# Optimization experiments

Measured on AMD Instinct MI355X. Metric: run time of the kernel, lower is better.

Reference implementation:

```python
import jax, jax.numpy as jnp
import numpy as np

B, LQ, LK = 8, 512, 512
DQ = DK = DV = 512
H = 128


def setup_inputs() -> dict:
    key = jax.random.key(0)
    kq, kk, kv, k1, k2, k3 = jax.random.split(key, 6)
    query = jax.random.normal(kq, (B, LQ, DQ), dtype=jnp.float32)
    key_t = jax.random.normal(kk, (B, LK, DK), dtype=jnp.float32)
    value = jax.random.normal(kv, (B, LK, DV), dtype=jnp.float32)
    # Linear weights stored torch-style as (out_features, in_features)
    w1 = jax.random.normal(k1, (H, DQ), dtype=jnp.float32) / np.sqrt(DQ)
    w2 = jax.random.normal(k2, (H, DK), dtype=jnp.float32) / np.sqrt(DK)
    v = jax.random.normal(k3, (1, H), dtype=jnp.float32) / np.sqrt(H)
    return {"query": query, "key": key_t, "value": value, "w1": w1, "w2": w2, "v": v}


def reference(query, key, value, w1, w2, v):
    # Linear projections first (mathematically identical to projecting the
    # broadcast tensors, since Linear is linear): (B,Lq,H), (B,Lk,H)
    q_proj = jnp.einsum("bqd,hd->bqh", query, w1)
    k_proj = jnp.einsum("bkd,hd->bkh", key, w2)
    # Broadcast add -> tanh -> project to scalar: (B,Lq,Lk,H) intermediate
    feat = jnp.tanh(q_proj[:, :, None, :] + k_proj[:, None, :, :])
    score = jnp.einsum("bqkh,h->bqk", feat, v[0])
    attention_weights = jax.nn.softmax(score, axis=-1)
    context_vector = jnp.einsum("bqk,bkv->bqv", attention_weights, value)
    return (attention_weights, context_vector)
```

## Files before the change

### kernel.cpp

```cpp
#include <hip/hip_runtime.h>

#define TWO_LOG2E 2.8853900817779268f

__device__ __forceinline__ float frcp(float x) {
#if __has_builtin(__builtin_amdgcn_rcpf)
  return __builtin_amdgcn_rcpf(x);
#else
  return 1.0f / x;
#endif
}
__device__ __forceinline__ float fexp2(float x) {
#if __has_builtin(__builtin_amdgcn_exp2f)
  return __builtin_amdgcn_exp2f(x);
#else
  return exp2f(x);
#endif
}
__device__ __forceinline__ unsigned short f2bf(float f) {
  unsigned int u = __float_as_uint(f);
  u += 0x7fffu + ((u >> 16) & 1u);
  return (unsigned short)(u >> 16);
}
__device__ __forceinline__ unsigned int pack2bf(float lo, float hi) {
  return (unsigned int)f2bf(lo) | ((unsigned int)f2bf(hi) << 16);
}

using short8 = __attribute__((ext_vector_type(8))) short;
using f32x4v = __attribute__((ext_vector_type(4))) float;
using f32x8s = __attribute__((ext_vector_type(8))) float;
using f32x2 = __attribute__((ext_vector_type(2))) float;

__device__ __forceinline__ f32x2 pkfma(f32x2 a, f32x2 b, f32x2 c) {
  return __builtin_elementwise_fma(a, b, c);
}
__device__ __forceinline__ f32x2 splat2(float x) {
  f32x2 r;
  r.x = x;
  r.y = x;
  return r;
}
__device__ __forceinline__ f32x2 unpack_bf2(unsigned u) {
  f32x2 r;
  r.x = __uint_as_float(u << 16);
  r.y = __uint_as_float(u & 0xffff0000u);
  return r;
}
__device__ __forceinline__ void cell4k(float a0, float a1, float a2, float a3,
                                       f32x2 b0, f32x2 b1, f32x2 b2, f32x2 b3,
                                       float v0, float v1, float v2, float v3,
                                       f32x2& s) {
  const f32x2 one = {1.f, 1.f};
  f32x2 x0 = pkfma(splat2(a0), b0, one);
  f32x2 x1 = pkfma(splat2(a1), b1, one);
  f32x2 x2 = pkfma(splat2(a2), b2, one);
  f32x2 x3 = pkfma(splat2(a3), b3, one);
  f32x2 p01 = x0 * x1, p23 = x2 * x3;
  f32x2 n01 = pkfma(splat2(v0), x1, splat2(v1) * x0);
  f32x2 n23 = pkfma(splat2(v2), x3, splat2(v3) * x2);
  f32x2 num = pkfma(n01, p23, n23 * p01);
  f32x2 den = p01 * p23;
  f32x2 r;
  r.x = frcp(den.x);
  r.y = frcp(den.y);
  s = pkfma(num, r, s);
}

__global__ __launch_bounds__(256) void k_pre(
    const float* __restrict__ query, const float* __restrict__ key,
    const float* __restrict__ w1, const float* __restrict__ w2,
    const float* __restrict__ value,
    float* __restrict__ Aout, unsigned short* __restrict__ BoutT,
    unsigned short* __restrict__ valT) {
  __shared__ __align__(16) char Abuf[16 * 128];
  __shared__ __align__(16) char Bbuf[128 * 128];
  __shared__ unsigned short ts[64][66];

  const int t = threadIdx.x;

  if (blockIdx.y == 0) {
    const int px = blockIdx.x;
    const bool isB = px >= 256;
    const float* in = isB ? key : query;
    const float* wm = isB ? w2 : w1;
    const int m0g = (px & 255) * 16;
    const int w = t >> 6, l = t & 63;

    f32x4v acc[2];
    acc[0] = 0;
    acc[1] = 0;

    float4 aS;
    float4 wS[4][2];

#define P_LOAD(k0_)                                                        \
  {                                                                        \
    aS = *(const float4*)&in[(m0g + (t >> 4)) * 512 + (k0_) + (t & 15) * 4]; \
    _Pragma("unroll") for (int i = 0; i < 4; ++i) {                        \
      int tt = t + i * 256;                                                \
      int row = tt >> 3, g = tt & 7;                                       \
      const float* src = &wm[row * 512 + (k0_) + g * 8];                   \
      wS[i][0] = *(const float4*)src;                                      \
      wS[i][1] = *(const float4*)(src + 4);                                \
    }                                                                      \
  }
#define P_WRITE()                                                          \
  {                                                                        \
    int arow = t >> 4, q4 = t & 15;                                        \
    *(uint2*)(Abuf + arow * 128 + (((q4 >> 1) ^ (arow & 7)) << 4) +        \
              ((q4 & 1) << 3)) =                                           \
        make_uint2(pack2bf(aS.x, aS.y), pack2bf(aS.z, aS.w));              \
    _Pragma("unroll") for (int i = 0; i < 4; ++i) {                        \
      int tt = t + i * 256;                                                \
      int row = tt >> 3, g = tt & 7;                                       \
      uint4 p = make_uint4(                                                \
          pack2bf(wS[i][0].x, wS[i][0].y), pack2bf(wS[i][0].z, wS[i][0].w),\
          pack2bf(wS[i][1].x, wS[i][1].y), pack2bf(wS[i][1].z, wS[i][1].w));\
      *(uint4*)(Bbuf + row * 128 + ((g ^ (row & 7)) << 4)) = p;            \
    }                                                                      \
  }

    P_LOAD(0);
#pragma unroll
    for (int ks8 = 0; ks8 < 8; ++ks8) {
      if (ks8) __syncthreads();
      P_WRITE();
      if (ks8 < 7) P_LOAD(ks8 * 64 + 64);
      __syncthreads();
#pragma unroll
      for (int ks = 0; ks < 2; ++ks) {
        const int gb = ks * 4 + (l >> 4);
        const int ra = l & 15;
        short8 af = *(const short8*)(Abuf + ra * 128 + ((gb ^ (ra & 7)) << 4));
#pragma unroll
        for (int ni = 0; ni < 2; ++ni) {
          const int rb = w * 32 + ni * 16 + (l & 15);
          short8 bf_ = *(const short8*)(Bbuf + rb * 128 + ((gb ^ (rb & 7)) << 4));
          if (isB)
            acc[ni] = __builtin_amdgcn_mfma_f32_16x16x32_bf16(bf_, af, acc[ni], 0, 0, 0);
          else
            acc[ni] = __builtin_amdgcn_mfma_f32_16x16x32_bf16(af, bf_, acc[ni], 0, 0, 0);
        }
      }
    }
#undef P_LOAD
#undef P_WRITE
    if (!isB) {
#pragma unroll
      for (int ni = 0; ni < 2; ++ni) {
        int col = w * 32 + ni * 16 + (l & 15);
#pragma unroll
        for (int j = 0; j < 4; ++j) {
          int row = m0g + (l >> 4) * 4 + j;
          Aout[row * 128 + col] = fexp2(acc[ni][j] * TWO_LOG2E);
        }
      }
    } else {
      int m = m0g + (l & 15);
#pragma unroll
      for (int ni = 0; ni < 2; ++ni)
#pragma unroll
        for (int j = 0; j < 4; ++j) {
          int h = w * 32 + ni * 16 + (l >> 4) * 4 + j;
          BoutT[h * 4096 + m] = f2bf(fexp2(acc[ni][j] * TWO_LOG2E));
        }
    }
  } else {
    const int x = blockIdx.x;
    const int b = x >> 6, k0 = ((x >> 3) & 7) * 64, n0 = (x & 7) * 64;
    {
      int kr = t >> 4, n4 = (t & 15) * 4;
#pragma unroll
      for (int i = 0; i < 4; ++i) {
        float4 f =
            *(const float4*)&value[((b * 512) + k0 + kr + 16 * i) * 512 + n0 + n4];
        *(ushort4*)&ts[kr + 16 * i][n4] =
            make_ushort4(f2bf(f.x), f2bf(f.y), f2bf(f.z), f2bf(f.w));
      }
    }
    __syncthreads();
    {
      int nw = t >> 4, k4 = (t & 15) * 4;
#pragma unroll
      for (int i = 0; i < 4; ++i) {
        int n = nw + 16 * i;
        ushort4 o = make_ushort4(ts[k4 + 0][n], ts[k4 + 1][n], ts[k4 + 2][n],
                                 ts[k4 + 3][n]);
        *(ushort4*)&valT[((b * 512) + n0 + n) * 512 + k0 + k4] = o;
      }
    }
  }
}

__global__ __launch_bounds__(256, 4) void k_score_softmax(
    const float* __restrict__ Aexp, const unsigned short* __restrict__ BexpT,
    const float* __restrict__ vw, float* __restrict__ attn) {
  __shared__ float red[4][4];

  const int tid = threadIdx.x;
  const int b = blockIdx.y;
  const int qbase = blockIdx.x * 4;
  const int wav = tid >> 6;
  const int lane = tid & 63;

  const unsigned* const bbase32 = (const unsigned*)(BexpT + b * 512);
  const int kidx = wav * 64 + lane;

  const float* const pa0 =
      Aexp + __builtin_amdgcn_readfirstlane((b * 512 + qbase) * 128);
  const float* const pa1 = pa0 + 128;
  const float* const pa2 = pa0 + 256;
  const float* const pa3 = pa0 + 384;
  const float* const pv = vw;

  f32x2 acc0 = {0.f, 0.f}, acc1 = {0.f, 0.f};
  f32x2 acc2 = {0.f, 0.f}, acc3 = {0.f, 0.f};

#pragma unroll
  for (int ch = 0; ch < 16; ++ch) {
    f32x8s sa0, sa1, sa2, sa3, sv;
    unsigned soff = (unsigned)(ch * 32);
    asm volatile(
        "s_load_dwordx8 %0, %5, %10\n\t"
        "s_load_dwordx8 %1, %6, %10\n\t"
        "s_load_dwordx8 %2, %7, %10\n\t"
        "s_load_dwordx8 %3, %8, %10\n\t"
        "s_load_dwordx8 %4, %9, %10"
        : "=&s"(sa0), "=&s"(sa1), "=&s"(sa2), "=&s"(sa3), "=&s"(sv)
        : "s"(pa0), "s"(pa1), "s"(pa2), "s"(pa3), "s"(pv), "s"(soff));

    unsigned u[8];
#pragma unroll
    for (int j = 0; j < 8; ++j)
      u[j] = bbase32[ch * 16384 + j * 2048 + kidx];

    asm volatile("s_waitcnt lgkmcnt(0)"
                 : "+s"(sa0), "+s"(sa1), "+s"(sa2), "+s"(sa3), "+s"(sv));

#pragma unroll
    for (int g = 0; g < 2; ++g) {
      f32x2 b0 = unpack_bf2(u[g * 4 + 0]);
      f32x2 b1 = unpack_bf2(u[g * 4 + 1]);
      f32x2 b2 = unpack_bf2(u[g * 4 + 2]);
      f32x2 b3 = unpack_bf2(u[g * 4 + 3]);
      const int h = g * 4;
      cell4k(sa0[h], sa0[h + 1], sa0[h + 2], sa0[h + 3], b0, b1, b2, b3,
             sv[h], sv[h + 1], sv[h + 2], sv[h + 3], acc0);
      cell4k(sa1[h], sa1[h + 1], sa1[h + 2], sa1[h + 3], b0, b1, b2, b3,
             sv[h], sv[h + 1], sv[h + 2], sv[h + 3], acc1);
      cell4k(sa2[h], sa2[h + 1], sa2[h + 2], sa2[h + 3], b0, b1, b2, b3,
             sv[h], sv[h + 1], sv[h + 2], sv[h + 3], acc2);
      cell4k(sa3[h], sa3[h + 1], sa3[h + 2], sa3[h + 3], b0, b1, b2, b3,
             sv[h], sv[h + 1], sv[h + 2], sv[h + 3], acc3);
    }
  }

  float P0e = fexp2(acc0.x * -TWO_LOG2E);
  float P0o = fexp2(acc0.y * -TWO_LOG2E);
  float P1e = fexp2(acc1.x * -TWO_LOG2E);
  float P1o = fexp2(acc1.y * -TWO_LOG2E);
  float P2e = fexp2(acc2.x * -TWO_LOG2E);
  float P2o = fexp2(acc2.y * -TWO_LOG2E);
  float P3e = fexp2(acc3.x * -TWO_LOG2E);
  float P3o = fexp2(acc3.y * -TWO_LOG2E);
  float s0 = P0e + P0o, s1 = P1e + P1o, s2 = P2e + P2o, s3 = P3e + P3o;
#pragma unroll
  for (int off = 32; off > 0; off >>= 1) {
    s0 += __shfl_xor(s0, off);
    s1 += __shfl_xor(s1, off);
    s2 += __shfl_xor(s2, off);
    s3 += __shfl_xor(s3, off);
  }
  if (lane == 0) {
    red[wav][0] = s0; red[wav][1] = s1; red[wav][2] = s2; red[wav][3] = s3;
  }
  __syncthreads();
  float r0 = frcp(red[0][0] + red[1][0] + red[2][0] + red[3][0]);
  float r1 = frcp(red[0][1] + red[1][1] + red[2][1] + red[3][1]);
  float r2 = frcp(red[0][2] + red[1][2] + red[2][2] + red[3][2]);
  float r3 = frcp(red[0][3] + red[1][3] + red[2][3] + red[3][3]);

  const int row0 = (b * 512 + qbase) * 512;
  const int k0 = kidx * 2;
  *(float2*)&attn[row0 + k0] = make_float2(P0e * r0, P0o * r0);
  *(float2*)&attn[row0 + 512 + k0] = make_float2(P1e * r1, P1o * r1);
  *(float2*)&attn[row0 + 1024 + k0] = make_float2(P2e * r2, P2o * r2);
  *(float2*)&attn[row0 + 1536 + k0] = make_float2(P3e * r3, P3o * r3);
}

__global__ __launch_bounds__(256) void k_context_mfma(
    const float* __restrict__ attn, const unsigned short* __restrict__ valT,
    float* __restrict__ ctx) {
  __shared__ __align__(16) char At[64 * 128];
  __shared__ __align__(16) char Bt[64 * 128];

  const int t = threadIdx.x;
  const int b = blockIdx.z;
  const int m0 = blockIdx.y * 64, n0 = blockIdx.x * 64;
  const int w = t >> 6, l = t & 63;
  const int wr = w >> 1, wc = w & 1;

  f32x4v acc[2][2];
  acc[0][0] = 0; acc[0][1] = 0; acc[1][0] = 0; acc[1][1] = 0;

  const int sr = t >> 2;
  const int sg = (t & 3);
  const int sswz = sr & 7;

  for (int k0 = 0; k0 < 512; k0 += 64) {
    if (k0) __syncthreads();
    {
      const float* src = &attn[(b * 512 + m0 + sr) * 512 + k0 + sg * 16];
      char* dst = At + sr * 128;
#pragma unroll
      for (int h = 0; h < 2; ++h) {
        float4 f0 = *(const float4*)(src + h * 8);
        float4 f1 = *(const float4*)(src + h * 8 + 4);
        uint4 p = make_uint4(pack2bf(f0.x, f0.y), pack2bf(f0.z, f0.w),
                             pack2bf(f1.x, f1.y), pack2bf(f1.z, f1.w));
        int g = sg * 2 + h;
        *(uint4*)(dst + ((g ^ sswz) << 4)) = p;
      }
      const unsigned short* srcb = &valT[(b * 512 + n0 + sr) * 512 + k0];
      char* dstb = Bt + sr * 128;
#pragma unroll
      for (int h = 0; h < 2; ++h) {
        int g = sg + h * 4;
        uint4 vb = *(const uint4*)(srcb + g * 8);
        *(uint4*)(dstb + ((g ^ sswz) << 4)) = vb;
      }
    }
    __syncthreads();
#pragma unroll
    for (int ks = 0; ks < 2; ++ks) {
      const int gb = ks * 4 + (l >> 4);
      short8 af[2], bf_[2];
#pragma unroll
      for (int mi = 0; mi < 2; ++mi) {
        int ra = wr * 32 + mi * 16 + (l & 15);
        af[mi] = *(const short8*)(At + ra * 128 + ((gb ^ (ra & 7)) << 4));
      }
#pragma unroll
      for (int ni = 0; ni < 2; ++ni) {
        int rb = wc * 32 + ni * 16 + (l & 15);
        bf_[ni] = *(const short8*)(Bt + rb * 128 + ((gb ^ (rb & 7)) << 4));
      }
#pragma unroll
      for (int mi = 0; mi < 2; ++mi)
#pragma unroll
        for (int ni = 0; ni < 2; ++ni)
          acc[mi][ni] = __builtin_amdgcn_mfma_f32_16x16x32_bf16(
              af[mi], bf_[ni], acc[mi][ni], 0, 0, 0);
    }
  }
  __syncthreads();
#pragma unroll
  for (int mi = 0; mi < 2; ++mi)
#pragma unroll
    for (int ni = 0; ni < 2; ++ni) {
      int col = n0 + wc * 32 + ni * 16 + (l & 15);
#pragma unroll
      for (int j = 0; j < 4; ++j) {
        int row = m0 + wr * 32 + mi * 16 + (l >> 4) * 4 + j;
        ctx[(b * 512 + row) * 512 + col] = acc[mi][ni][j];
      }
    }
}

extern "C" void kernel_launch(void* const* d_in, const int* in_sizes, int n_in,
                              void* d_out, int out_size, void* d_ws, size_t ws_size,
                              hipStream_t stream) {
  const float* query = (const float*)d_in[0];
  const float* key   = (const float*)d_in[1];
  const float* value = (const float*)d_in[2];
  const float* w1    = (const float*)d_in[3];
  const float* w2    = (const float*)d_in[4];
  const float* v     = (const float*)d_in[5];

  float* attn = (float*)d_out;
  float* ctx  = attn + 8 * 512 * 512;

  float* Aexp = (float*)d_ws;
  unsigned short* BexpT = (unsigned short*)(Aexp + 4096 * 128);
  unsigned short* valT = BexpT + 128 * 4096;

  k_pre<<<dim3(512, 2), 256, 0, stream>>>(query, key, w1, w2, value,
                                          Aexp, BexpT, valT);
  k_score_softmax<<<dim3(128, 8), 256, 0, stream>>>(Aexp, BexpT, v, attn);
  k_context_mfma<<<dim3(8, 8, 8), 256, 0, stream>>>(attn, valT, ctx);
}
```

Baseline: 60.35 us.

## Split score kernel's hidden-dim reduction across two wave groups per block

The score/softmax kernel now launches 512 threads per block. Two groups of four waves each reduce half of the 128 hidden dimensions, then the partial sums are combined through shared memory. Each group writes two of the four query rows. This halves the serial per-thread accumulation chain and doubles resident waves to hide memory latency. The cost is an extra LDS exchange, a barrier, redundant exp work, and tighter register limits under the new launch bounds.

```diff
diff --git a/kernel.cpp b/kernel.cpp
--- a/kernel.cpp
+++ b/kernel.cpp
@@ -191,19 +191,22 @@
   }
 }
 
-__global__ __launch_bounds__(256, 4) void k_score_softmax(
+__global__ __launch_bounds__(512, 8) void k_score_softmax(
     const float* __restrict__ Aexp, const unsigned short* __restrict__ BexpT,
     const float* __restrict__ vw, float* __restrict__ attn) {
-  __shared__ float red[4][4];
+  __shared__ __align__(16) f32x2 part[512][4];
+  __shared__ float red[8][4];
 
   const int tid = threadIdx.x;
   const int b = blockIdx.y;
   const int qbase = blockIdx.x * 4;
   const int wav = tid >> 6;
+  const int hgrp = wav >> 2;
+  const int kq = wav & 3;
   const int lane = tid & 63;
 
   const unsigned* const bbase32 = (const unsigned*)(BexpT + b * 512);
-  const int kidx = wav * 64 + lane;
+  const int kidx = kq * 64 + lane;
 
   const float* const pa0 =
       Aexp + __builtin_amdgcn_readfirstlane((b * 512 + qbase) * 128);
@@ -211,14 +214,15 @@
   const float* const pa2 = pa0 + 256;
   const float* const pa3 = pa0 + 384;
   const float* const pv = vw;
+  const unsigned hoff = (unsigned)__builtin_amdgcn_readfirstlane(hgrp * 256);
 
   f32x2 acc0 = {0.f, 0.f}, acc1 = {0.f, 0.f};
   f32x2 acc2 = {0.f, 0.f}, acc3 = {0.f, 0.f};
 
 #pragma unroll
-  for (int ch = 0; ch < 16; ++ch) {
+  for (int ch = 0; ch < 8; ++ch) {
     f32x8s sa0, sa1, sa2, sa3, sv;
-    unsigned soff = (unsigned)(ch * 32);
+    unsigned soff = hoff + (unsigned)(ch * 32);
     asm volatile(
         "s_load_dwordx8 %0, %5, %10\n\t"
         "s_load_dwordx8 %1, %6, %10\n\t"
@@ -231,7 +235,7 @@
     unsigned u[8];
 #pragma unroll
     for (int j = 0; j < 8; ++j)
-      u[j] = bbase32[ch * 16384 + j * 2048 + kidx];
+      u[j] = bbase32[hgrp * 131072 + ch * 16384 + j * 2048 + kidx];
 
     asm volatile("s_waitcnt lgkmcnt(0)"
                  : "+s"(sa0), "+s"(sa1), "+s"(sa2), "+s"(sa3), "+s"(sv));
@@ -254,6 +258,19 @@
     }
   }
 
+  part[tid][0] = acc0;
+  part[tid][1] = acc1;
+  part[tid][2] = acc2;
+  part[tid][3] = acc3;
+  __syncthreads();
+  {
+    const f32x2* pp = part[tid ^ 256];
+    acc0 += pp[0];
+    acc1 += pp[1];
+    acc2 += pp[2];
+    acc3 += pp[3];
+  }
+
   float P0e = fexp2(acc0.x * -TWO_LOG2E);
   float P0o = fexp2(acc0.y * -TWO_LOG2E);
   float P1e = fexp2(acc1.x * -TWO_LOG2E);
@@ -274,17 +291,21 @@
     red[wav][0] = s0; red[wav][1] = s1; red[wav][2] = s2; red[wav][3] = s3;
   }
   __syncthreads();
-  float r0 = frcp(red[0][0] + red[1][0] + red[2][0] + red[3][0]);
-  float r1 = frcp(red[0][1] + red[1][1] + red[2][1] + red[3][1]);
-  float r2 = frcp(red[0][2] + red[1][2] + red[2][2] + red[3][2]);
-  float r3 = frcp(red[0][3] + red[1][3] + red[2][3] + red[3][3]);
+  const int rb = hgrp * 4;
+  float r0 = frcp(red[rb][0] + red[rb + 1][0] + red[rb + 2][0] + red[rb + 3][0]);
+  float r1 = frcp(red[rb][1] + red[rb + 1][1] + red[rb + 2][1] + red[rb + 3][1]);
+  float r2 = frcp(red[rb][2] + red[rb + 1][2] + red[rb + 2][2] + red[rb + 3][2]);
+  float r3 = frcp(red[rb][3] + red[rb + 1][3] + red[rb + 2][3] + red[rb + 3][3]);
 
   const int row0 = (b * 512 + qbase) * 512;
   const int k0 = kidx * 2;
-  *(float2*)&attn[row0 + k0] = make_float2(P0e * r0, P0o * r0);
-  *(float2*)&attn[row0 + 512 + k0] = make_float2(P1e * r1, P1o * r1);
-  *(float2*)&attn[row0 + 1024 + k0] = make_float2(P2e * r2, P2o * r2);
-  *(float2*)&attn[row0 + 1536 + k0] = make_float2(P3e * r3, P3o * r3);
+  if (hgrp == 0) {
+    *(float2*)&attn[row0 + k0] = make_float2(P0e * r0, P0o * r0);
+    *(float2*)&attn[row0 + 512 + k0] = make_float2(P1e * r1, P1o * r1);
+  } else {
+    *(float2*)&attn[row0 + 1024 + k0] = make_float2(P2e * r2, P2o * r2);
+    *(float2*)&attn[row0 + 1536 + k0] = make_float2(P3e * r3, P3o * r3);
+  }
 }
 
 __global__ __launch_bounds__(256) void k_context_mfma(
@@ -385,6 +406,6 @@
 
   k_pre<<<dim3(512, 2), 256, 0, stream>>>(query, key, w1, w2, value,
                                           Aexp, BexpT, valT);
-  k_score_softmax<<<dim3(128, 8), 256, 0, stream>>>(Aexp, BexpT, v, attn);
+  k_score_softmax<<<dim3(128, 8), 512, 0, stream>>>(Aexp, BexpT, v, attn);
   k_context_mfma<<<dim3(8, 8, 8), 256, 0, stream>>>(attn, valT, ctx);
 }
```

Result: no change. 60.11 us (-0.4%).
